# Performance work log

Measured on AMD Instinct MI355X. Metric: run time of the kernel, lower is better.

Reference implementation:

```python
import jax, jax.numpy as jnp
import numpy as np

N = 4_194_304  # number of sample points


def _make_C():
    # Faithful reproduction of the module's compliance matrix (including the
    # asymmetry: Ci[2,0]=Ci[2,1]=-vp, NOT -vp/Ep, exactly as in the source).
    vp, Ep = 0.4, 0.21
    Ci = np.zeros((6, 6), dtype=np.float64)
    Ci[0, 0] = 1 / Ep;  Ci[0, 1] = -vp / Ep; Ci[0, 2] = -vp / Ep
    Ci[1, 0] = -vp / Ep; Ci[1, 1] = 1 / Ep;  Ci[1, 2] = -vp / Ep
    Ci[2, 0] = -vp;      Ci[2, 1] = -vp;     Ci[2, 2] = 1 / Ep
    Ci[3, 3] = 2 * (1 + vp) / Ep
    Ci[4, 4] = 2 * (1 + vp) / Ep
    Ci[5, 5] = 2 * (1 + vp) / Ep
    return jnp.asarray(np.linalg.inv(Ci), dtype=jnp.float32)

_C = _make_C()  # [6, 6] stiffness matrix


def setup_inputs() -> dict:
    key = jax.random.key(0)
    k1, k2, k3, k4 = jax.random.split(key, 4)
    return {
        "grad_u": jax.random.normal(k1, (N, 3), dtype=jnp.float32),
        "grad_v": jax.random.normal(k2, (N, 3), dtype=jnp.float32),
        "grad_w": jax.random.normal(k3, (N, 3), dtype=jnp.float32),
        "gt_sdf": jax.random.normal(k4, (N,), dtype=jnp.float32),
    }


def reference(grad_u, grad_v, grad_w, gt_sdf):
    # Build per-point strain tensor in Voigt-like notation: [N, 6]
    et = jnp.stack([
        grad_u[:, 0],
        grad_v[:, 1],
        grad_w[:, 2],
        (grad_u[:, 1] + grad_v[:, 0]) * 0.5,
        (grad_u[:, 2] + grad_w[:, 0]) * 0.5,
        (grad_w[:, 1] + grad_v[:, 2]) * 0.5,
    ], axis=1)
    # Per-point quadratic form et_i^T C et_i == diag(et @ C @ et.T) without the
    # O(N^2) intermediate the torch code materializes.
    q = jnp.einsum('ni,ij,nj->n', et, _C, et)
    # Mask = points with gt_sdf < 1e-8 (index_select in torch; masked here so
    # shapes stay static under jit). Excluded points contribute 0 to the norm.
    mask = gt_sdf < 1e-8
    qm = jnp.where(mask, q, 0.0)
    count = jnp.sum(mask).astype(et.dtype)  # et.shape[0] after index_select
    W = jnp.sqrt(jnp.sum(qm * qm))           # L2 norm of the diagonal vector
    return W / count
```

## Files before the change

kernel.cpp:

```cpp
#include <hip/hip_runtime.h>
#include <math.h>

struct CParams {
    float b[3][3];
    float s;
};

static CParams make_C() {
    const double vp = 0.4, Ep = 0.21;
    double A[3][3] = {
        {1.0 / Ep, -vp / Ep, -vp / Ep},
        {-vp / Ep, 1.0 / Ep, -vp / Ep},
        {-vp,      -vp,      1.0 / Ep},
    };
    double inv[3][3] = {{1, 0, 0}, {0, 1, 0}, {0, 0, 1}};
    for (int col = 0; col < 3; ++col) {
        int piv = col;
        for (int r = col + 1; r < 3; ++r)
            if (fabs(A[r][col]) > fabs(A[piv][col])) piv = r;
        if (piv != col) {
            for (int c = 0; c < 3; ++c) {
                double t = A[col][c]; A[col][c] = A[piv][c]; A[piv][c] = t;
                t = inv[col][c]; inv[col][c] = inv[piv][c]; inv[piv][c] = t;
            }
        }
        double d = A[col][col];
        for (int c = 0; c < 3; ++c) { A[col][c] /= d; inv[col][c] /= d; }
        for (int r = 0; r < 3; ++r) {
            if (r == col) continue;
            double f = A[r][col];
            for (int c = 0; c < 3; ++c) {
                A[r][c] -= f * A[col][c];
                inv[r][c] -= f * inv[col][c];
            }
        }
    }
    CParams p;
    for (int i = 0; i < 3; ++i)
        for (int j = 0; j < 3; ++j)
            p.b[i][j] = (float)inv[i][j];
    p.s = (float)(Ep / (2.0 * (1.0 + vp)));
    return p;
}

static const CParams g_C = make_C();

#define MAXB 2048

__device__ __forceinline__ void accum_packet(
    const float4* u4, const float4* v4, const float4* w4, const float4* s4,
    int p, const CParams& C, float& sumq2, float& cnt)
{
    float4 ua = u4[3 * p], ub = u4[3 * p + 1], uc = u4[3 * p + 2];
    float4 va = v4[3 * p], vb = v4[3 * p + 1], vc = v4[3 * p + 2];
    float4 wa = w4[3 * p], wb = w4[3 * p + 1], wc = w4[3 * p + 2];
    float4 g  = s4[p];

    float uu[12] = {ua.x, ua.y, ua.z, ua.w, ub.x, ub.y, ub.z, ub.w,
                    uc.x, uc.y, uc.z, uc.w};
    float vv[12] = {va.x, va.y, va.z, va.w, vb.x, vb.y, vb.z, vb.w,
                    vc.x, vc.y, vc.z, vc.w};
    float ww[12] = {wa.x, wa.y, wa.z, wa.w, wb.x, wb.y, wb.z, wb.w,
                    wc.x, wc.y, wc.z, wc.w};
    float gg[4] = {g.x, g.y, g.z, g.w};

#pragma unroll
    for (int k = 0; k < 4; ++k) {
        float e0 = uu[3 * k + 0];
        float e1 = vv[3 * k + 1];
        float e2 = ww[3 * k + 2];
        float e3 = 0.5f * (uu[3 * k + 1] + vv[3 * k + 0]);
        float e4 = 0.5f * (uu[3 * k + 2] + ww[3 * k + 0]);
        float e5 = 0.5f * (ww[3 * k + 1] + vv[3 * k + 2]);

        float q = e0 * (C.b[0][0] * e0 + C.b[0][1] * e1 + C.b[0][2] * e2)
                + e1 * (C.b[1][0] * e0 + C.b[1][1] * e1 + C.b[1][2] * e2)
                + e2 * (C.b[2][0] * e0 + C.b[2][1] * e1 + C.b[2][2] * e2)
                + C.s * (e3 * e3 + e4 * e4 + e5 * e5);

        bool m = gg[k] < 1e-8f;
        float qm = m ? q : 0.0f;
        sumq2 += qm * qm;
        cnt   += m ? 1.0f : 0.0f;
    }
}

__global__ __launch_bounds__(256) void biomech_reduce(
    const float* __restrict__ gu, const float* __restrict__ gv,
    const float* __restrict__ gw, const float* __restrict__ gs,
    float* __restrict__ ws, int npack, int n, CParams C)
{
    const float4* u4 = (const float4*)gu;
    const float4* v4 = (const float4*)gv;
    const float4* w4 = (const float4*)gw;
    const float4* s4 = (const float4*)gs;

    float sumq2 = 0.0f;
    float cnt   = 0.0f;

    const int t = blockIdx.x * blockDim.x + threadIdx.x;
    const int T = gridDim.x * blockDim.x;

    for (int base = 0; base < npack; base += 2 * T) {
        int p0 = base + t;
        int p1 = p0 + T;
        if (p1 < npack) {
            accum_packet(u4, v4, w4, s4, p0, C, sumq2, cnt);
            accum_packet(u4, v4, w4, s4, p1, C, sumq2, cnt);
        } else {
            if (p0 < npack) accum_packet(u4, v4, w4, s4, p0, C, sumq2, cnt);
        }
    }

    if (blockIdx.x == 0 && threadIdx.x == 0) {
        for (int i = npack * 4; i < n; ++i) {
            float e0 = gu[3 * i + 0];
            float e1 = gv[3 * i + 1];
            float e2 = gw[3 * i + 2];
            float e3 = 0.5f * (gu[3 * i + 1] + gv[3 * i + 0]);
            float e4 = 0.5f * (gu[3 * i + 2] + gw[3 * i + 0]);
            float e5 = 0.5f * (gw[3 * i + 1] + gv[3 * i + 2]);
            float q = e0 * (C.b[0][0] * e0 + C.b[0][1] * e1 + C.b[0][2] * e2)
                    + e1 * (C.b[1][0] * e0 + C.b[1][1] * e1 + C.b[1][2] * e2)
                    + e2 * (C.b[2][0] * e0 + C.b[2][1] * e1 + C.b[2][2] * e2)
                    + C.s * (e3 * e3 + e4 * e4 + e5 * e5);
            bool m = gs[i] < 1e-8f;
            float qm = m ? q : 0.0f;
            sumq2 += qm * qm;
            cnt   += m ? 1.0f : 0.0f;
        }
    }

#pragma unroll
    for (int off = 32; off > 0; off >>= 1) {
        sumq2 += __shfl_down(sumq2, off);
        cnt   += __shfl_down(cnt, off);
    }

    __shared__ float ssum[4], scnt[4];
    const int wave = threadIdx.x >> 6;
    const int lane = threadIdx.x & 63;
    if (lane == 0) { ssum[wave] = sumq2; scnt[wave] = cnt; }
    __syncthreads();
    if (threadIdx.x == 0) {
        float s2 = 0.0f, c2 = 0.0f;
#pragma unroll
        for (int i = 0; i < 4; ++i) { s2 += ssum[i]; c2 += scnt[i]; }
        ws[blockIdx.x]        = s2;
        ws[MAXB + blockIdx.x] = c2;
    }
}

__global__ __launch_bounds__(256) void biomech_finalize(
    const float* __restrict__ ws, float* __restrict__ out, int nb)
{
    float s = 0.0f, c = 0.0f;
    for (int i = threadIdx.x; i < nb; i += 256) {
        s += ws[i];
        c += ws[MAXB + i];
    }
#pragma unroll
    for (int off = 32; off > 0; off >>= 1) {
        s += __shfl_down(s, off);
        c += __shfl_down(c, off);
    }
    __shared__ float ssum[4], scnt[4];
    const int wave = threadIdx.x >> 6;
    const int lane = threadIdx.x & 63;
    if (lane == 0) { ssum[wave] = s; scnt[wave] = c; }
    __syncthreads();
    if (threadIdx.x == 0) {
        float s2 = ssum[0] + ssum[1] + ssum[2] + ssum[3];
        float c2 = scnt[0] + scnt[1] + scnt[2] + scnt[3];
        out[0] = sqrtf(s2) / c2;
    }
}

extern "C" void kernel_launch(void* const* d_in, const int* in_sizes, int n_in,
                              void* d_out, int out_size, void* d_ws, size_t ws_size,
                              hipStream_t stream) {
    const float* gu = (const float*)d_in[0];
    const float* gv = (const float*)d_in[1];
    const float* gw = (const float*)d_in[2];
    const float* gs = (const float*)d_in[3];
    float* ws = (float*)d_ws;
    float* out = (float*)d_out;

    const int n = in_sizes[3];
    const int npack = n / 4;

    const int block = 256;
    int grid = (npack + block - 1) / block;
    if (grid > MAXB) grid = MAXB;
    while (grid > 1 && (size_t)(MAXB + grid) * sizeof(float) > ws_size) grid >>= 1;
    if (grid < 1) grid = 1;

    biomech_reduce<<<grid, block, 0, stream>>>(gu, gv, gw, gs, ws, npack, n, g_C);
    biomech_finalize<<<1, block, 0, stream>>>(ws, out, grid);
}
```

Baseline: 178.7 us.

## Stage AoS gradients through LDS with coalesced loads and register prefetch

```diff
diff --git a/kernel.cpp b/kernel.cpp
--- a/kernel.cpp
+++ b/kernel.cpp
@@ -46,74 +46,114 @@
 static const CParams g_C = make_C();
 
 #define MAXB 2048
-
-__device__ __forceinline__ void accum_packet(
-    const float4* u4, const float4* v4, const float4* w4, const float4* s4,
-    int p, const CParams& C, float& sumq2, float& cnt)
-{
-    float4 ua = u4[3 * p], ub = u4[3 * p + 1], uc = u4[3 * p + 2];
-    float4 va = v4[3 * p], vb = v4[3 * p + 1], vc = v4[3 * p + 2];
-    float4 wa = w4[3 * p], wb = w4[3 * p + 1], wc = w4[3 * p + 2];
-    float4 g  = s4[p];
-
-    float uu[12] = {ua.x, ua.y, ua.z, ua.w, ub.x, ub.y, ub.z, ub.w,
-                    uc.x, uc.y, uc.z, uc.w};
-    float vv[12] = {va.x, va.y, va.z, va.w, vb.x, vb.y, vb.z, vb.w,
-                    vc.x, vc.y, vc.z, vc.w};
-    float ww[12] = {wa.x, wa.y, wa.z, wa.w, wb.x, wb.y, wb.z, wb.w,
-                    wc.x, wc.y, wc.z, wc.w};
-    float gg[4] = {g.x, g.y, g.z, g.w};
-
-#pragma unroll
-    for (int k = 0; k < 4; ++k) {
-        float e0 = uu[3 * k + 0];
-        float e1 = vv[3 * k + 1];
-        float e2 = ww[3 * k + 2];
-        float e3 = 0.5f * (uu[3 * k + 1] + vv[3 * k + 0]);
-        float e4 = 0.5f * (uu[3 * k + 2] + ww[3 * k + 0]);
-        float e5 = 0.5f * (ww[3 * k + 1] + vv[3 * k + 2]);
-
-        float q = e0 * (C.b[0][0] * e0 + C.b[0][1] * e1 + C.b[0][2] * e2)
-                + e1 * (C.b[1][0] * e0 + C.b[1][1] * e1 + C.b[1][2] * e2)
-                + e2 * (C.b[2][0] * e0 + C.b[2][1] * e1 + C.b[2][2] * e2)
-                + C.s * (e3 * e3 + e4 * e4 + e5 * e5);
-
-        bool m = gg[k] < 1e-8f;
-        float qm = m ? q : 0.0f;
-        sumq2 += qm * qm;
-        cnt   += m ? 1.0f : 0.0f;
-    }
-}
-
-__global__ __launch_bounds__(256) void biomech_reduce(
+#define TPB  256
+#define TILE 256
+#define F4A  192
+
+#define ZERO4 make_float4(0.0f, 0.0f, 0.0f, 0.0f)
+
+__global__ __launch_bounds__(TPB) void biomech_reduce(
     const float* __restrict__ gu, const float* __restrict__ gv,
     const float* __restrict__ gw, const float* __restrict__ gs,
-    float* __restrict__ ws, int npack, int n, CParams C)
+    float* __restrict__ ws, int n, CParams C)
 {
+    __shared__ float4 buf[TPB / 64][3][F4A];
+
+    const int wave    = threadIdx.x >> 6;
+    const int lane    = threadIdx.x & 63;
+    const int nwaves  = gridDim.x * (TPB / 64);
+    const int ngroups = n / TILE;
+
     const float4* u4 = (const float4*)gu;
     const float4* v4 = (const float4*)gv;
     const float4* w4 = (const float4*)gw;
-    const float4* s4 = (const float4*)gs;
-
-    float sumq2 = 0.0f;
-    float cnt   = 0.0f;
-
-    const int t = blockIdx.x * blockDim.x + threadIdx.x;
-    const int T = gridDim.x * blockDim.x;
-
-    for (int base = 0; base < npack; base += 2 * T) {
-        int p0 = base + t;
-        int p1 = p0 + T;
-        if (p1 < npack) {
-            accum_packet(u4, v4, w4, s4, p0, C, sumq2, cnt);
-            accum_packet(u4, v4, w4, s4, p1, C, sumq2, cnt);
-        } else {
-            if (p0 < npack) accum_packet(u4, v4, w4, s4, p0, C, sumq2, cnt);
-        }
+
+    float sumq2 = 0.0f, cnt = 0.0f;
+
+    float4 pu0 = ZERO4, pu1 = ZERO4, pu2 = ZERO4;
+    float4 pv0 = ZERO4, pv1 = ZERO4, pv2 = ZERO4;
+    float4 pw0 = ZERO4, pw1 = ZERO4, pw2 = ZERO4;
+    float  ps0 = 1.0f, ps1 = 1.0f, ps2 = 1.0f, ps3 = 1.0f;
+
+    {
+        const int g = blockIdx.x * (TPB / 64) + wave;
+        if (g < ngroups) {
+            const int b  = g * F4A;
+            const int sb = g * TILE;
+            pu0 = u4[b + lane]; pu1 = u4[b + 64 + lane]; pu2 = u4[b + 128 + lane];
+            pv0 = v4[b + lane]; pv1 = v4[b + 64 + lane]; pv2 = v4[b + 128 + lane];
+            pw0 = w4[b + lane]; pw1 = w4[b + 64 + lane]; pw2 = w4[b + 128 + lane];
+            ps0 = gs[sb + lane];       ps1 = gs[sb + 64 + lane];
+            ps2 = gs[sb + 128 + lane]; ps3 = gs[sb + 192 + lane];
+        }
+    }
+
+    for (int gb = blockIdx.x * (TPB / 64); gb < ngroups; gb += nwaves) {
+        const int g  = gb + wave;
+        const int gn = g + nwaves;
+
+        float4 nu0 = ZERO4, nu1 = ZERO4, nu2 = ZERO4;
+        float4 nv0 = ZERO4, nv1 = ZERO4, nv2 = ZERO4;
+        float4 nw0 = ZERO4, nw1 = ZERO4, nw2 = ZERO4;
+        float  ns0 = 1.0f, ns1 = 1.0f, ns2 = 1.0f, ns3 = 1.0f;
+        if (gn < ngroups) {
+            const int b  = gn * F4A;
+            const int sb = gn * TILE;
+            nu0 = u4[b + lane]; nu1 = u4[b + 64 + lane]; nu2 = u4[b + 128 + lane];
+            nv0 = v4[b + lane]; nv1 = v4[b + 64 + lane]; nv2 = v4[b + 128 + lane];
+            nw0 = w4[b + lane]; nw1 = w4[b + 64 + lane]; nw2 = w4[b + 128 + lane];
+            ns0 = gs[sb + lane];       ns1 = gs[sb + 64 + lane];
+            ns2 = gs[sb + 128 + lane]; ns3 = gs[sb + 192 + lane];
+        }
+
+        if (g < ngroups) {
+            buf[wave][0][lane] = pu0; buf[wave][0][64 + lane] = pu1; buf[wave][0][128 + lane] = pu2;
+            buf[wave][1][lane] = pv0; buf[wave][1][64 + lane] = pv1; buf[wave][1][128 + lane] = pv2;
+            buf[wave][2][lane] = pw0; buf[wave][2][64 + lane] = pw1; buf[wave][2][128 + lane] = pw2;
+        }
+
+        __syncthreads();
+
+        if (g < ngroups) {
+            const float* bu = (const float*)&buf[wave][0][0];
+            const float* bv = (const float*)&buf[wave][1][0];
+            const float* bw = (const float*)&buf[wave][2][0];
+            const float sd[4] = {ps0, ps1, ps2, ps3};
+
+#pragma unroll
+            for (int k = 0; k < 4; ++k) {
+                const int p = lane + (k << 6);
+                float u0 = bu[3 * p], u1 = bu[3 * p + 1], u2 = bu[3 * p + 2];
+                float v0 = bv[3 * p], v1 = bv[3 * p + 1], v2 = bv[3 * p + 2];
+                float w0 = bw[3 * p], w1 = bw[3 * p + 1], w2 = bw[3 * p + 2];
+
+                float e0 = u0, e1 = v1, e2 = w2;
+                float e3 = 0.5f * (u1 + v0);
+                float e4 = 0.5f * (u2 + w0);
+                float e5 = 0.5f * (w1 + v2);
+
+                float q = e0 * (C.b[0][0] * e0 + C.b[0][1] * e1 + C.b[0][2] * e2)
+                        + e1 * (C.b[1][0] * e0 + C.b[1][1] * e1 + C.b[1][2] * e2)
+                        + e2 * (C.b[2][0] * e0 + C.b[2][1] * e1 + C.b[2][2] * e2)
+                        + C.s * (e3 * e3 + e4 * e4 + e5 * e5);
+
+                bool m = sd[k] < 1e-8f;
+                float qm = m ? q : 0.0f;
+                sumq2 += qm * qm;
+                cnt   += m ? 1.0f : 0.0f;
+            }
+        }
+
+        __syncthreads();
+
+        pu0 = nu0; pu1 = nu1; pu2 = nu2;
+        pv0 = nv0; pv1 = nv1; pv2 = nv2;
+        pw0 = nw0; pw1 = nw1; pw2 = nw2;
+        ps0 = ns0; ps1 = ns1; ps2 = ns2; ps3 = ns3;
     }
 
     if (blockIdx.x == 0 && threadIdx.x == 0) {
-        for (int i = npack * 4; i < n; ++i) {
+        for (int i = (n / TILE) * TILE; i < n; ++i) {
             float e0 = gu[3 * i + 0];
             float e1 = gv[3 * i + 1];
             float e2 = gw[3 * i + 2];
@@ -138,8 +178,6 @@
     }
 
     __shared__ float ssum[4], scnt[4];
-    const int wave = threadIdx.x >> 6;
-    const int lane = threadIdx.x & 63;
     if (lane == 0) { ssum[wave] = sumq2; scnt[wave] = cnt; }
     __syncthreads();
     if (threadIdx.x == 0) {
@@ -187,14 +225,15 @@
     float* out = (float*)d_out;
 
     const int n = in_sizes[3];
-    const int npack = n / 4;
-
-    const int block = 256;
-    int grid = (npack + block - 1) / block;
+    const int ngroups = n / TILE;
+    const int wpb = TPB / 64;
+
+    int grid = (ngroups + wpb - 1) / wpb;
+    if (grid > 1024) grid = 1024;
     if (grid > MAXB) grid = MAXB;
     while (grid > 1 && (size_t)(MAXB + grid) * sizeof(float) > ws_size) grid >>= 1;
     if (grid < 1) grid = 1;
 
-    biomech_reduce<<<grid, block, 0, stream>>>(gu, gv, gw, gs, ws, npack, n, g_C);
-    biomech_finalize<<<1, block, 0, stream>>>(ws, out, grid);
-}
+    biomech_reduce<<<grid, TPB, 0, stream>>>(gu, gv, gw, gs, ws, n, g_C);
+    biomech_finalize<<<1, 256, 0, stream>>>(ws, out, grid);
+}
```

New measurement: 178.2 us. About the same (-0.3%).
